# Optimization experiments

Hardware: AMD Instinct MI355X
Metric: run time of the kernel (lower is better)

The kernel has to match this reference:

```python
import jax, jax.numpy as jnp
import numpy as np

NEG = jnp.float32(-1e30)  # log-semiring 'zero' (avoid -inf for safe grads)


def _ctc_total_scores(log_probs, targets, input_lengths, target_lengths):
    """Log-semiring forward over the composed CTC topology.

    log_probs: (T, N, C) log-softmax outputs, blank id = 0
    targets:   (N*L,) flat labels in [1, C)
    Returns tot_scores (N,): log p(targets | log_probs) per utterance,
    identical to k2.intersect_dense + get_tot_scores(log_semiring=True).
    """
    T, N, C = log_probs.shape
    L = targets.shape[0] // N
    tgt = targets.reshape(N, L).astype(jnp.int32)
    S = 2 * L + 1  # extended sequence: blank y1 blank y2 ... yL blank

    ext = jnp.zeros((N, S), jnp.int32).at[:, 1::2].set(tgt)
    s_idx = jnp.arange(S)
    # skip transition s-2 -> s allowed only for label states with ext[s] != ext[s-2]
    diff = jnp.concatenate([jnp.zeros((N, 2), bool), ext[:, 2:] != ext[:, :-2]], axis=1)
    skip_ok = (s_idx[None, :] % 2 == 1) & (s_idx[None, :] >= 2) & diff
    # states beyond this utterance's extended length are invalid
    valid = s_idx[None, :] <= 2 * target_lengths.astype(jnp.int32)[:, None]
    s_end = 2 * target_lengths.astype(jnp.int32)  # index of final blank state

    def emit(lp):  # (N, C) -> (N, S): gather log-probs of extended labels
        return jnp.take_along_axis(lp, ext, axis=1)

    e0 = emit(log_probs[0])
    a0 = jnp.full((N, S), NEG).at[:, 0].set(e0[:, 0]).at[:, 1].set(e0[:, 1])
    a0 = jnp.where(valid, a0, NEG)

    def final_score(a):  # logsumexp over the two accepting states
        last = jnp.take_along_axis(a, s_end[:, None], axis=1)[:, 0]
        prev = jnp.take_along_axis(a, (s_end - 1)[:, None], axis=1)[:, 0]
        return jnp.logaddexp(last, prev)

    def step(a, lp):
        sh1 = jnp.concatenate([jnp.full((N, 1), NEG), a[:, :-1]], axis=1)
        sh2 = jnp.concatenate([jnp.full((N, 2), NEG), a[:, :-2]], axis=1)
        sh2 = jnp.where(skip_ok, sh2, NEG)
        a_new = jnp.logaddexp(jnp.logaddexp(a, sh1), sh2) + emit(lp)
        a_new = jnp.where(valid, a_new, NEG)
        return a_new, final_score(a_new)

    _, finals = jax.lax.scan(step, a0, log_probs[1:])  # finals: (T-1, N)
    finals = jnp.concatenate([final_score(a0)[None], finals], axis=0)  # (T, N)
    tot = jnp.take_along_axis(finals, (input_lengths.astype(jnp.int32) - 1)[None, :], axis=0)[0]
    return tot


def setup_inputs() -> dict:
    key = jax.random.key(0)
    k1, k2_ = jax.random.split(key)
    T, N, C, L = 1500, 32, 1024, 100
    log_probs = jax.nn.log_softmax(
        jax.random.normal(k1, (T, N, C), dtype=jnp.float32), axis=-1)
    targets = jax.random.randint(k2_, (N * L,), 1, C, dtype=jnp.int32)  # no blanks
    input_lengths = jnp.full((N,), T, dtype=jnp.int32)
    target_lengths = jnp.full((N,), L, dtype=jnp.int32)
    return {"log_probs": log_probs, "targets": targets,
            "input_lengths": input_lengths, "target_lengths": target_lengths}


def reference(log_probs, targets, input_lengths, target_lengths):
    tot = _ctc_total_scores(log_probs, targets, input_lengths, target_lengths)
    # drop -inf (failed) segments like get_tot_objf_and_num_frames, then negate sum
    finite = tot > jnp.float32(-1e29)
    return -jnp.sum(jnp.where(finite, tot, 0.0))
```

## Files before the change

kernel.cpp:

```cpp
#include <hip/hip_runtime.h>
#include <stdint.h>

#define NEGF  (-1e30f)
#define LOG2E 1.4426950408889634f
#define LN2F  0.6931471805599453f

__device__ __forceinline__ float fexp2(float x) {
#if __has_builtin(__builtin_amdgcn_exp2f)
    return __builtin_amdgcn_exp2f(x);
#else
    return exp2f(x);
#endif
}
__device__ __forceinline__ float flog2(float x) {
#if __has_builtin(__builtin_amdgcn_logf)
    return __builtin_amdgcn_logf(x);
#else
    return log2f(x);
#endif
}
__device__ __forceinline__ float lse2(float a, float b) {
    float m  = fmaxf(a, b);
    float mn = fminf(a, b);
    return m + flog2(1.0f + fexp2(mn - m));
}
__device__ __forceinline__ float lse3(float a, float b, float c) {
    float m = fmaxf(fmaxf(a, b), c);
    float s = fexp2(a - m) + fexp2(b - m) + fexp2(c - m);
    return m + flog2(s);
}

__device__ __forceinline__ float dpp_shr1(float x, float fill) {
    int r = __builtin_amdgcn_update_dpp(__float_as_int(fill), __float_as_int(x),
                                        0x138, 0xf, 0xf, false);
    return __int_as_float(r);
}
__device__ __forceinline__ float dpp_shl1(float x, float fill) {
    int r = __builtin_amdgcn_update_dpp(__float_as_int(fill), __float_as_int(x),
                                        0x130, 0xf, 0xf, false);
    return __int_as_float(r);
}

#define RB  16
#define VMW "s_waitcnt vmcnt(52)"

__device__ __forceinline__ void stage_row(const float* __restrict__ src, float* dst)
{
    const int lane = threadIdx.x;
    const float* g = src + (lane << 2);
    __builtin_amdgcn_global_load_lds((const __attribute__((address_space(1))) void*)(g),
        (__attribute__((address_space(3))) void*)(dst), 16, 0, 0);
    __builtin_amdgcn_global_load_lds((const __attribute__((address_space(1))) void*)(g + 256),
        (__attribute__((address_space(3))) void*)(dst + 256), 16, 0, 0);
    __builtin_amdgcn_global_load_lds((const __attribute__((address_space(1))) void*)(g + 512),
        (__attribute__((address_space(3))) void*)(dst + 512), 16, 0, 0);
    __builtin_amdgcn_global_load_lds((const __attribute__((address_space(1))) void*)(g + 768),
        (__attribute__((address_space(3))) void*)(dst + 768), 16, 0, 0);
}

__device__ __forceinline__ void lds_read3(uint32_t sb, uint32_t o1, uint32_t o3,
                                          float& eb, float& e1, float& e3)
{
    asm volatile("s_mov_b32 m0, -1\n\t"
                 "ds_read_b32 %0, %3\n\t"
                 "ds_read_b32 %1, %4\n\t"
                 "ds_read_b32 %2, %5"
                 : "=&v"(eb), "=&v"(e1), "=&v"(e3)
                 : "v"(sb), "v"(sb + o1), "v"(sb + o3)
                 : "memory");
}
__device__ __forceinline__ void lds_read4(uint32_t sb, uint32_t o1, uint32_t o3, uint32_t o5,
                                          float& eb, float& e1, float& e3, float& e5)
{
    asm volatile("s_mov_b32 m0, -1\n\t"
                 "ds_read_b32 %0, %4\n\t"
                 "ds_read_b32 %1, %5\n\t"
                 "ds_read_b32 %2, %6\n\t"
                 "ds_read_b32 %3, %7"
                 : "=&v"(eb), "=&v"(e1), "=&v"(e3), "=&v"(e5)
                 : "v"(sb), "v"(sb + o1), "v"(sb + o3), "v"(sb + o5)
                 : "memory");
}

#define LGKM_WAIT3(c, x0, x1, x2) \
    asm volatile("s_waitcnt lgkmcnt(" #c ")" : "+v"(x0), "+v"(x1), "+v"(x2) :: "memory")
#define LGKM_WAIT4(c, x0, x1, x2, x3) \
    asm volatile("s_waitcnt lgkmcnt(" #c ")" : "+v"(x0), "+v"(x1), "+v"(x2), "+v"(x3) :: "memory")

__global__ __launch_bounds__(64, 1)
void ctc_scan(const float* __restrict__ lp, const int* __restrict__ tgt,
              const int* __restrict__ ilen, const int* __restrict__ tlen,
              float* __restrict__ wsA, float* __restrict__ wsB,
              int T, int N, int C, int L)
{
    __shared__ float ring[RB * 1024];

    const int  b      = blockIdx.x;
    const bool is_fwd = (b < N);
    const int  n      = is_fwd ? b : (b - N);
    const int  lane   = threadIdx.x;
    const int  len_t  = tlen[n];
    const int  len_in = ilen[n];
    const int  tm     = (len_in - 1) >> 1;
    const int  send   = 2 * len_t;

    const long tb = (long)n * L;
    auto getT = [&](int k) -> int {
        return (k >= 0 && k < len_t) ? tgt[tb + k] : 0;
    };
    const int lm1 = getT(2 * lane - 1);
    const int l1  = getT(2 * lane);
    const int l2  = getT(2 * lane + 1);
    const int l3  = getT(2 * lane + 2);
    const uint32_t o1 = (uint32_t)l1 << 2;
    const uint32_t o3 = (uint32_t)l2 << 2;
    const uint32_t o5 = (uint32_t)l3 << 2;
    const bool skip1 = (lane > 0) && (l1 != lm1);
    const bool skip3 = (l2 != l1);
    const bool skip5 = (l3 != l2);
    const int  s0 = 4 * lane;

    const long   rstride = (long)N * C;
    const float* row0    = lp + (long)n * C;
    const uint32_t ringb =
        (uint32_t)(uintptr_t)(const __attribute__((address_space(3))) void*)ring;


    if (is_fwd) {
        float eb0 = row0[0];
        float e10 = row0[l1];
        asm volatile("s_waitcnt vmcnt(0)" : "+v"(eb0), "+v"(e10) :: "memory");
        float a0 = (lane == 0) ? eb0 * LOG2E : NEGF;
        float a1 = (lane == 0 && 1 <= send) ? e10 * LOG2E : NEGF;
        float a2 = NEGF, a3 = NEGF;
        float p3 = NEGF;

        auto fstep = [&](float ebr, float e1r, float e3r) {
            float eb = ebr * LOG2E, e1 = e1r * LOG2E, e3 = e3r * LOG2E;
            float n0 = lse2(a0, p3) + eb;
            float n1 = lse3(a1, a0, skip1 ? p3 : NEGF) + e1;
            float n2 = lse2(a2, a1) + eb;
            float n3 = lse3(a3, a2, skip3 ? a1 : NEGF) + e3;
            a0 = n0; a1 = n1; a2 = n2; a3 = n3;
            p3 = dpp_shr1(a3, NEGF);
        };

        const int nsteps = tm;
        const int lim    = len_in - 1;
        for (int j = 0; j < RB - 1; ++j) {
            int r = 1 + j; if (r > lim) r = lim;
            stage_row(row0 + (long)r * rstride, ring + (j << 10));
        }
        asm volatile(VMW ::: "memory");
        float ebA, e1A, e3A, ebB, e1B, e3B;
        lds_read3(ringb,        o1, o3, ebA, e1A, e3A);
        lds_read3(ringb + 4096, o1, o3, ebB, e1B, e3B);

        int i = 0;
        for (; i + 1 < nsteps; i += 2) {
            {   int s = i + RB - 1; int r = s + 1; if (r > lim) r = lim;
                stage_row(row0 + (long)r * rstride, ring + ((s & (RB - 1)) << 10)); }
            LGKM_WAIT3(3, ebA, e1A, e3A);
            fstep(ebA, e1A, e3A);
            asm volatile(VMW ::: "memory");
            lds_read3(ringb + (uint32_t)(((i + 2) & (RB - 1)) << 12), o1, o3,
                      ebA, e1A, e3A);

            {   int s = i + RB; int r = s + 1; if (r > lim) r = lim;
                stage_row(row0 + (long)r * rstride, ring + ((s & (RB - 1)) << 10)); }
            LGKM_WAIT3(3, ebB, e1B, e3B);
            fstep(ebB, e1B, e3B);
            asm volatile(VMW ::: "memory");
            lds_read3(ringb + (uint32_t)(((i + 3) & (RB - 1)) << 12), o1, o3,
                      ebB, e1B, e3B);
        }
        if (i < nsteps) {
            LGKM_WAIT3(0, ebA, e1A, e3A);
            fstep(ebA, e1A, e3A);
        }
        asm volatile("s_waitcnt vmcnt(0) lgkmcnt(0)" ::: "memory");
        *((float4*)(wsA + (long)n * 256) + lane) = make_float4(a0, a1, a2, a3);
    } else {
        float b0 = (s0     == send || s0     == send - 1) ? 0.0f : NEGF;
        float b1 = (s0 + 1 == send || s0 + 1 == send - 1) ? 0.0f : NEGF;
        float b2 = (s0 + 2 == send || s0 + 2 == send - 1) ? 0.0f : NEGF;
        float b3 = (s0 + 3 == send || s0 + 3 == send - 1) ? 0.0f : NEGF;
        float q0 = dpp_shl1(b0, NEGF);
        float q1 = dpp_shl1(b1, NEGF);

        auto bstep = [&](float ebr, float e1r, float e3r, float e5r) {
            float ebl = ebr * LOG2E, e1l = e1r * LOG2E;
            float e3l = e3r * LOG2E, e5l = e5r * LOG2E;
            float f0 = b0 + ebl;
            float f1 = b1 + e1l;
            float f2 = b2 + ebl;
            float f3 = b3 + e3l;
            float f0p = q0 + ebl;
            float f1p = q1 + e5l;
            b0 = lse2(f0, f1);
            b1 = lse3(f1, f2, skip3 ? f3 : NEGF);
            b2 = lse2(f2, f3);
            b3 = lse3(f3, f0p, skip5 ? f1p : NEGF);
            q0 = dpp_shl1(b0, NEGF);
            q1 = dpp_shl1(b1, NEGF);
        };

        const int nsteps = len_in - 1 - tm;
        asm volatile("s_waitcnt vmcnt(0)" ::: "memory");
        for (int j = 0; j < RB - 1; ++j) {
            int r = len_in - 1 - j; if (r < 0) r = 0;
            stage_row(row0 + (long)r * rstride, ring + (j << 10));
        }
        asm volatile(VMW ::: "memory");
        float ebA, e1A, e3A, e5A, ebB, e1B, e3B, e5B;
        lds_read4(ringb,        o1, o3, o5, ebA, e1A, e3A, e5A);
        lds_read4(ringb + 4096, o1, o3, o5, ebB, e1B, e3B, e5B);

        int i = 0;
        for (; i + 1 < nsteps; i += 2) {
            {   int s = i + RB - 1; int r = len_in - 1 - s; if (r < 0) r = 0;
                stage_row(row0 + (long)r * rstride, ring + ((s & (RB - 1)) << 10)); }
            LGKM_WAIT4(4, ebA, e1A, e3A, e5A);
            bstep(ebA, e1A, e3A, e5A);
            asm volatile(VMW ::: "memory");
            lds_read4(ringb + (uint32_t)(((i + 2) & (RB - 1)) << 12), o1, o3, o5,
                      ebA, e1A, e3A, e5A);

            {   int s = i + RB; int r = len_in - 1 - s; if (r < 0) r = 0;
                stage_row(row0 + (long)r * rstride, ring + ((s & (RB - 1)) << 10)); }
            LGKM_WAIT4(4, ebB, e1B, e3B, e5B);
            bstep(ebB, e1B, e3B, e5B);
            asm volatile(VMW ::: "memory");
            lds_read4(ringb + (uint32_t)(((i + 3) & (RB - 1)) << 12), o1, o3, o5,
                      ebB, e1B, e3B, e5B);
        }
        if (i < nsteps) {
            LGKM_WAIT4(0, ebA, e1A, e3A, e5A);
            bstep(ebA, e1A, e3A, e5A);
        }
        asm volatile("s_waitcnt vmcnt(0) lgkmcnt(0)" ::: "memory");
        *((float4*)(wsB + (long)n * 256) + lane) = make_float4(b0, b1, b2, b3);
    }
}

__global__ __launch_bounds__(64, 1)
void ctc_combine(const float* __restrict__ wsA, const float* __restrict__ wsB,
                 float* __restrict__ out)
{
    const int n = blockIdx.x;
    const int lane = threadIdx.x;
    const float4 A = *((const float4*)(wsA + (long)n * 256) + lane);
    const float4 B = *((const float4*)(wsB + (long)n * 256) + lane);
    float v = lse2(lse2(A.x + B.x, A.y + B.y), lse2(A.z + B.z, A.w + B.w));
    #pragma unroll
    for (int off = 1; off < 64; off <<= 1) {
        float o = __shfl_xor(v, off, 64);
        v = lse2(v, o);
    }
    if (lane == 0) {
        float tot = v * LN2F;
        if (tot > -1e29f) atomicAdd(out, -tot);
    }
}

extern "C" void kernel_launch(void* const* d_in, const int* in_sizes, int n_in,
                              void* d_out, int out_size, void* d_ws, size_t ws_size,
                              hipStream_t stream) {
    const float* lp      = (const float*)d_in[0];
    const int*   targets = (const int*)d_in[1];
    const int*   in_len  = (const int*)d_in[2];
    const int*   tgt_len = (const int*)d_in[3];
    const int N = in_sizes[2];
    const int L = in_sizes[1] / N;
    const int C = 1024;
    const int T = (int)((long)in_sizes[0] / ((long)N * C));

    float* out = (float*)d_out;
    float* wsA = (float*)d_ws;
    float* wsB = wsA + (long)N * 256;

    hipMemsetAsync(out, 0, sizeof(float), stream);
    ctc_scan<<<2 * N, 64, 0, stream>>>(lp, targets, in_len, tgt_len,
                                       wsA, wsB, T, N, C, L);
    ctc_combine<<<N, 64, 0, stream>>>(wsA, wsB, out);
}
```

Measured before the change: 336.6 us.

## Switch CTC scan from log-domain to scaled linear-domain recurrence with periodic renorm

Replaces the per-step log-sum-exp recurrences with linear-probability arithmetic. Emissions are normalised by the blank emission, the blank log-probs are accumulated in double, and the state is rescaled every 8 steps with per-lane power-of-two exponent tracking passed across lanes via DPP. This removes most exp/log transcendentals from the serial critical path. The ring pipeline is also deepened to four LDS reads in flight, with a 16-step unroll and an adjusted vmcnt threshold. The trade-off is more complex exponent bookkeeping and a risk of underflow or precision loss between renormalisations.

```diff
diff --git a/kernel.cpp b/kernel.cpp
--- a/kernel.cpp
+++ b/kernel.cpp
@@ -24,11 +24,6 @@
     float mn = fminf(a, b);
     return m + flog2(1.0f + fexp2(mn - m));
 }
-__device__ __forceinline__ float lse3(float a, float b, float c) {
-    float m = fmaxf(fmaxf(a, b), c);
-    float s = fexp2(a - m) + fexp2(b - m) + fexp2(c - m);
-    return m + flog2(s);
-}
 
 __device__ __forceinline__ float dpp_shr1(float x, float fill) {
     int r = __builtin_amdgcn_update_dpp(__float_as_int(fill), __float_as_int(x),
@@ -42,9 +37,9 @@
 }
 
 #define RB  16
-#define VMW "s_waitcnt vmcnt(52)"
-
-__device__ __forceinline__ void stage_row(const float* __restrict__ src, float* dst)
+#define VMW "s_waitcnt vmcnt(44)"
+
+__device__ __forceinline__ void stage_row_c(const float* src, float* dst)
 {
     const int lane = threadIdx.x;
     const float* g = src + (lane << 2);
@@ -86,6 +81,24 @@
     asm volatile("s_waitcnt lgkmcnt(" #c ")" : "+v"(x0), "+v"(x1), "+v"(x2) :: "memory")
 #define LGKM_WAIT4(c, x0, x1, x2, x3) \
     asm volatile("s_waitcnt lgkmcnt(" #c ")" : "+v"(x0), "+v"(x1), "+v"(x2), "+v"(x3) :: "memory")
+
+#define RENORM_LANE(x0, x1, x2, x3, DPPC)                                     \
+  do {                                                                        \
+    float m_ = fmaxf(fmaxf(x0, x1), fmaxf(x2, x3));                           \
+    int   ei_ = (__float_as_int(m_) >> 23) & 0xff;                            \
+    bool  z_  = (m_ == 0.0f);                                                 \
+    float sc_ = z_ ? 1.0f : ((ei_ != 0) ? __int_as_float((254 - ei_) << 23)   \
+                                        : __int_as_float(253 << 23));         \
+    int   d_  = z_ ? 0 : ((ei_ != 0) ? (ei_ - 127) : -126);                   \
+    int   eu_ = esum + d_;                                                    \
+    int   en_ = __builtin_amdgcn_update_dpp(eu_, eu_, (DPPC), 0xf, 0xf, false);\
+    esum = z_ ? en_ : eu_;                          \
+    x0 *= sc_; x1 *= sc_; x2 *= sc_; x3 *= sc_;                               \
+    int   ep_ = __builtin_amdgcn_update_dpp(esum, esum, (DPPC), 0xf, 0xf, false);\
+    int   ce_ = ep_ - esum;                                                   \
+    ce_ = ce_ < -126 ? -126 : (ce_ > 126 ? 126 : ce_);                        \
+    cross = __int_as_float((ce_ + 127) << 23);                                \
+  } while (0)
 
 __global__ __launch_bounds__(64, 1)
 void ctc_scan(const float* __restrict__ lp, const int* __restrict__ tgt,
@@ -125,121 +138,192 @@
     const uint32_t ringb =
         (uint32_t)(uintptr_t)(const __attribute__((address_space(3))) void*)ring;
 
+    int    esum  = 0;
+    float  cross = 1.0f;
+    double dsum  = 0.0;
 
     if (is_fwd) {
         float eb0 = row0[0];
         float e10 = row0[l1];
         asm volatile("s_waitcnt vmcnt(0)" : "+v"(eb0), "+v"(e10) :: "memory");
-        float a0 = (lane == 0) ? eb0 * LOG2E : NEGF;
-        float a1 = (lane == 0 && 1 <= send) ? e10 * LOG2E : NEGF;
-        float a2 = NEGF, a3 = NEGF;
-        float p3 = NEGF;
-
-        auto fstep = [&](float ebr, float e1r, float e3r) {
-            float eb = ebr * LOG2E, e1 = e1r * LOG2E, e3 = e3r * LOG2E;
-            float n0 = lse2(a0, p3) + eb;
-            float n1 = lse3(a1, a0, skip1 ? p3 : NEGF) + e1;
-            float n2 = lse2(a2, a1) + eb;
-            float n3 = lse3(a3, a2, skip3 ? a1 : NEGF) + e3;
-            a0 = n0; a1 = n1; a2 = n2; a3 = n3;
-            p3 = dpp_shr1(a3, NEGF);
-        };
+        dsum = (double)eb0;
+        float a0 = (lane == 0) ? 1.0f : 0.0f;
+        float a1 = (lane == 0 && 1 <= send) ? fexp2((e10 - eb0) * LOG2E) : 0.0f;
+        float a2 = 0.0f, a3 = 0.0f;
+        float p3 = 0.0f;
 
         const int nsteps = tm;
         const int lim    = len_in - 1;
         for (int j = 0; j < RB - 1; ++j) {
             int r = 1 + j; if (r > lim) r = lim;
-            stage_row(row0 + (long)r * rstride, ring + (j << 10));
-        }
+            stage_row_c(row0 + (long)r * rstride, ring + (j << 10));
+        }
+        int rr = (16 > lim) ? lim : 16;
+        const float* pstage = row0 + (long)rr * rstride;
+
         asm volatile(VMW ::: "memory");
-        float ebA, e1A, e3A, ebB, e1B, e3B;
-        lds_read3(ringb,        o1, o3, ebA, e1A, e3A);
-        lds_read3(ringb + 4096, o1, o3, ebB, e1B, e3B);
+        float rb0, r1_0, r3_0, rb1, r1_1, r3_1;
+        float rb2, r1_2, r3_2, rb3, r1_3, r3_3;
+        lds_read3(ringb,         o1, o3, rb0, r1_0, r3_0);
+        lds_read3(ringb + 4096,  o1, o3, rb1, r1_1, r3_1);
+        lds_read3(ringb + 8192,  o1, o3, rb2, r1_2, r3_2);
+        lds_read3(ringb + 12288, o1, o3, rb3, r1_3, r3_3);
+
+#define FSLOT(u, s)                                                            \
+  do {                                                                         \
+    stage_row_c(pstage, ring + ((((u) + 15) & 15) << 10));                     \
+    { int adv = (rr < lim); rr += adv; pstage += adv ? rstride : 0; }          \
+    asm volatile(VMW ::: "memory");                                            \
+    LGKM_WAIT3(9, rb##s, r1_##s, r3_##s);                                      \
+    float cb = rb##s, c1v = r1_##s, c3v = r3_##s;                              \
+    lds_read3(ringb + ((((u) + 4) & 15) << 12), o1, o3, rb##s, r1_##s, r3_##s);\
+    float rv1 = fexp2((c1v - cb) * LOG2E);                                     \
+    float rv3 = fexp2((c3v - cb) * LOG2E);                                     \
+    dsum += (double)cb;                                                        \
+    float n0 = a0 + p3;                                                        \
+    float n1 = (a1 + a0 + (skip1 ? p3 : 0.0f)) * rv1;                          \
+    float n2 = a2 + a1;                                                        \
+    float n3 = (a3 + a2 + (skip3 ? a1 : 0.0f)) * rv3;                          \
+    a0 = n0; a1 = n1; a2 = n2; a3 = n3;                                        \
+    p3 = dpp_shr1(a3, 0.0f) * cross;                                           \
+  } while (0)
+
+#define RENORM_F() do { RENORM_LANE(a0, a1, a2, a3, 0x138);                    \
+                        p3 = dpp_shr1(a3, 0.0f) * cross; } while (0)
 
         int i = 0;
-        for (; i + 1 < nsteps; i += 2) {
-            {   int s = i + RB - 1; int r = s + 1; if (r > lim) r = lim;
-                stage_row(row0 + (long)r * rstride, ring + ((s & (RB - 1)) << 10)); }
-            LGKM_WAIT3(3, ebA, e1A, e3A);
-            fstep(ebA, e1A, e3A);
-            asm volatile(VMW ::: "memory");
-            lds_read3(ringb + (uint32_t)(((i + 2) & (RB - 1)) << 12), o1, o3,
-                      ebA, e1A, e3A);
-
-            {   int s = i + RB; int r = s + 1; if (r > lim) r = lim;
-                stage_row(row0 + (long)r * rstride, ring + ((s & (RB - 1)) << 10)); }
-            LGKM_WAIT3(3, ebB, e1B, e3B);
-            fstep(ebB, e1B, e3B);
-            asm volatile(VMW ::: "memory");
-            lds_read3(ringb + (uint32_t)(((i + 3) & (RB - 1)) << 12), o1, o3,
-                      ebB, e1B, e3B);
-        }
-        if (i < nsteps) {
-            LGKM_WAIT3(0, ebA, e1A, e3A);
-            fstep(ebA, e1A, e3A);
-        }
-        asm volatile("s_waitcnt vmcnt(0) lgkmcnt(0)" ::: "memory");
-        *((float4*)(wsA + (long)n * 256) + lane) = make_float4(a0, a1, a2, a3);
+        while (i + 16 <= nsteps) {
+            FSLOT(0,0);  FSLOT(1,1);  FSLOT(2,2);  FSLOT(3,3);
+            FSLOT(4,0);  FSLOT(5,1);  FSLOT(6,2);  FSLOT(7,3);
+            RENORM_F();
+            FSLOT(8,0);  FSLOT(9,1);  FSLOT(10,2); FSLOT(11,3);
+            FSLOT(12,0); FSLOT(13,1); FSLOT(14,2); FSLOT(15,3);
+            RENORM_F();
+            i += 16;
+        }
+        asm volatile("s_waitcnt vmcnt(0) lgkmcnt(0)"
+                     :: "v"(rb0), "v"(r1_0), "v"(r3_0), "v"(rb1), "v"(r1_1), "v"(r3_1),
+                        "v"(rb2), "v"(r1_2), "v"(r3_2), "v"(rb3), "v"(r1_3), "v"(r3_3)
+                     : "memory");
+        for (; i < nsteps; ++i) {
+            float cb, c1v, c3v;
+            lds_read3(ringb + (uint32_t)((i & 15) << 12), o1, o3, cb, c1v, c3v);
+            LGKM_WAIT3(0, cb, c1v, c3v);
+            float rv1 = fexp2((c1v - cb) * LOG2E);
+            float rv3 = fexp2((c3v - cb) * LOG2E);
+            dsum += (double)cb;
+            float n0 = a0 + p3;
+            float n1 = (a1 + a0 + (skip1 ? p3 : 0.0f)) * rv1;
+            float n2 = a2 + a1;
+            float n3 = (a3 + a2 + (skip3 ? a1 : 0.0f)) * rv3;
+            a0 = n0; a1 = n1; a2 = n2; a3 = n3;
+            p3 = dpp_shr1(a3, 0.0f) * cross;
+            if ((i & 7) == 7) RENORM_F();
+        }
+        float S  = (float)(dsum * 1.4426950408889634);
+        float fe = (float)esum;
+        float w0 = fmaxf(flog2(a0) + fe + S, NEGF);
+        float w1 = fmaxf(flog2(a1) + fe + S, NEGF);
+        float w2 = fmaxf(flog2(a2) + fe + S, NEGF);
+        float w3 = fmaxf(flog2(a3) + fe + S, NEGF);
+        *((float4*)(wsA + (long)n * 256) + lane) = make_float4(w0, w1, w2, w3);
+#undef FSLOT
+#undef RENORM_F
     } else {
-        float b0 = (s0     == send || s0     == send - 1) ? 0.0f : NEGF;
-        float b1 = (s0 + 1 == send || s0 + 1 == send - 1) ? 0.0f : NEGF;
-        float b2 = (s0 + 2 == send || s0 + 2 == send - 1) ? 0.0f : NEGF;
-        float b3 = (s0 + 3 == send || s0 + 3 == send - 1) ? 0.0f : NEGF;
-        float q0 = dpp_shl1(b0, NEGF);
-        float q1 = dpp_shl1(b1, NEGF);
-
-        auto bstep = [&](float ebr, float e1r, float e3r, float e5r) {
-            float ebl = ebr * LOG2E, e1l = e1r * LOG2E;
-            float e3l = e3r * LOG2E, e5l = e5r * LOG2E;
-            float f0 = b0 + ebl;
-            float f1 = b1 + e1l;
-            float f2 = b2 + ebl;
-            float f3 = b3 + e3l;
-            float f0p = q0 + ebl;
-            float f1p = q1 + e5l;
-            b0 = lse2(f0, f1);
-            b1 = lse3(f1, f2, skip3 ? f3 : NEGF);
-            b2 = lse2(f2, f3);
-            b3 = lse3(f3, f0p, skip5 ? f1p : NEGF);
-            q0 = dpp_shl1(b0, NEGF);
-            q1 = dpp_shl1(b1, NEGF);
-        };
+        float b0 = (s0     == send || s0     == send - 1) ? 1.0f : 0.0f;
+        float b1 = (s0 + 1 == send || s0 + 1 == send - 1) ? 1.0f : 0.0f;
+        float b2 = (s0 + 2 == send || s0 + 2 == send - 1) ? 1.0f : 0.0f;
+        float b3 = (s0 + 3 == send || s0 + 3 == send - 1) ? 1.0f : 0.0f;
+        float q0 = dpp_shl1(b0, 0.0f);
+        float q1 = dpp_shl1(b1, 0.0f);
 
         const int nsteps = len_in - 1 - tm;
-        asm volatile("s_waitcnt vmcnt(0)" ::: "memory");
         for (int j = 0; j < RB - 1; ++j) {
             int r = len_in - 1 - j; if (r < 0) r = 0;
-            stage_row(row0 + (long)r * rstride, ring + (j << 10));
-        }
+            stage_row_c(row0 + (long)r * rstride, ring + (j << 10));
+        }
+        int rr = len_in - 16; if (rr < 0) rr = 0;
+        const float* pstage = row0 + (long)rr * rstride;
+
         asm volatile(VMW ::: "memory");
-        float ebA, e1A, e3A, e5A, ebB, e1B, e3B, e5B;
-        lds_read4(ringb,        o1, o3, o5, ebA, e1A, e3A, e5A);
-        lds_read4(ringb + 4096, o1, o3, o5, ebB, e1B, e3B, e5B);
+        float rb0, r1_0, r3_0, r5_0, rb1, r1_1, r3_1, r5_1;
+        float rb2, r1_2, r3_2, r5_2, rb3, r1_3, r3_3, r5_3;
+        lds_read4(ringb,         o1, o3, o5, rb0, r1_0, r3_0, r5_0);
+        lds_read4(ringb + 4096,  o1, o3, o5, rb1, r1_1, r3_1, r5_1);
+        lds_read4(ringb + 8192,  o1, o3, o5, rb2, r1_2, r3_2, r5_2);
+        lds_read4(ringb + 12288, o1, o3, o5, rb3, r1_3, r3_3, r5_3);
+
+#define BSLOT(u, s)                                                            \
+  do {                                                                         \
+    stage_row_c(pstage, ring + ((((u) + 15) & 15) << 10));                     \
+    { int adv = (rr > 0); rr -= adv; pstage -= adv ? rstride : 0; }            \
+    asm volatile(VMW ::: "memory");                                            \
+    LGKM_WAIT4(12, rb##s, r1_##s, r3_##s, r5_##s);                             \
+    float cb = rb##s, c1v = r1_##s, c3v = r3_##s, c5v = r5_##s;                \
+    lds_read4(ringb + ((((u) + 4) & 15) << 12), o1, o3, o5,                    \
+              rb##s, r1_##s, r3_##s, r5_##s);                                  \
+    float rv1 = fexp2((c1v - cb) * LOG2E);                                     \
+    float rv3 = fexp2((c3v - cb) * LOG2E);                                     \
+    float rv5 = fexp2((c5v - cb) * LOG2E);                                     \
+    dsum += (double)cb;                                                        \
+    float g1 = b1 * rv1, g3 = b3 * rv3;                                        \
+    float n0 = b0 + g1;                                                        \
+    float n1 = g1 + b2 + (skip3 ? g3 : 0.0f);                                  \
+    float n2 = b2 + g3;                                                        \
+    float n3 = g3 + q0 + (skip5 ? q1 * rv5 : 0.0f);                            \
+    b0 = n0; b1 = n1; b2 = n2; b3 = n3;                                        \
+    q0 = dpp_shl1(b0, 0.0f) * cross;                                           \
+    q1 = dpp_shl1(b1, 0.0f) * cross;                                           \
+  } while (0)
+
+#define RENORM_B() do { RENORM_LANE(b0, b1, b2, b3, 0x130);                    \
+                        q0 = dpp_shl1(b0, 0.0f) * cross;                       \
+                        q1 = dpp_shl1(b1, 0.0f) * cross; } while (0)
 
         int i = 0;
-        for (; i + 1 < nsteps; i += 2) {
-            {   int s = i + RB - 1; int r = len_in - 1 - s; if (r < 0) r = 0;
-                stage_row(row0 + (long)r * rstride, ring + ((s & (RB - 1)) << 10)); }
-            LGKM_WAIT4(4, ebA, e1A, e3A, e5A);
-            bstep(ebA, e1A, e3A, e5A);
-            asm volatile(VMW ::: "memory");
-            lds_read4(ringb + (uint32_t)(((i + 2) & (RB - 1)) << 12), o1, o3, o5,
-                      ebA, e1A, e3A, e5A);
-
-            {   int s = i + RB; int r = len_in - 1 - s; if (r < 0) r = 0;
-                stage_row(row0 + (long)r * rstride, ring + ((s & (RB - 1)) << 10)); }
-            LGKM_WAIT4(4, ebB, e1B, e3B, e5B);
-            bstep(ebB, e1B, e3B, e5B);
-            asm volatile(VMW ::: "memory");
-            lds_read4(ringb + (uint32_t)(((i + 3) & (RB - 1)) << 12), o1, o3, o5,
-                      ebB, e1B, e3B, e5B);
-        }
-        if (i < nsteps) {
-            LGKM_WAIT4(0, ebA, e1A, e3A, e5A);
-            bstep(ebA, e1A, e3A, e5A);
-        }
-        asm volatile("s_waitcnt vmcnt(0) lgkmcnt(0)" ::: "memory");
-        *((float4*)(wsB + (long)n * 256) + lane) = make_float4(b0, b1, b2, b3);
+        while (i + 16 <= nsteps) {
+            BSLOT(0,0);  BSLOT(1,1);  BSLOT(2,2);  BSLOT(3,3);
+            BSLOT(4,0);  BSLOT(5,1);  BSLOT(6,2);  BSLOT(7,3);
+            RENORM_B();
+            BSLOT(8,0);  BSLOT(9,1);  BSLOT(10,2); BSLOT(11,3);
+            BSLOT(12,0); BSLOT(13,1); BSLOT(14,2); BSLOT(15,3);
+            RENORM_B();
+            i += 16;
+        }
+        asm volatile("s_waitcnt vmcnt(0) lgkmcnt(0)"
+                     :: "v"(rb0), "v"(r1_0), "v"(r3_0), "v"(r5_0),
+                        "v"(rb1), "v"(r1_1), "v"(r3_1), "v"(r5_1),
+                        "v"(rb2), "v"(r1_2), "v"(r3_2), "v"(r5_2),
+                        "v"(rb3), "v"(r1_3), "v"(r3_3), "v"(r5_3)
+                     : "memory");
+        for (; i < nsteps; ++i) {
+            float cb, c1v, c3v, c5v;
+            lds_read4(ringb + (uint32_t)((i & 15) << 12), o1, o3, o5,
+                      cb, c1v, c3v, c5v);
+            LGKM_WAIT4(0, cb, c1v, c3v, c5v);
+            float rv1 = fexp2((c1v - cb) * LOG2E);
+            float rv3 = fexp2((c3v - cb) * LOG2E);
+            float rv5 = fexp2((c5v - cb) * LOG2E);
+            dsum += (double)cb;
+            float g1 = b1 * rv1, g3 = b3 * rv3;
+            float n0 = b0 + g1;
+            float n1 = g1 + b2 + (skip3 ? g3 : 0.0f);
+            float n2 = b2 + g3;
+            float n3 = g3 + q0 + (skip5 ? q1 * rv5 : 0.0f);
+            b0 = n0; b1 = n1; b2 = n2; b3 = n3;
+            q0 = dpp_shl1(b0, 0.0f) * cross;
+            q1 = dpp_shl1(b1, 0.0f) * cross;
+            if ((i & 7) == 7) RENORM_B();
+        }
+        float S  = (float)(dsum * 1.4426950408889634);
+        float fe = (float)esum;
+        float w0 = fmaxf(flog2(b0) + fe + S, NEGF);
+        float w1 = fmaxf(flog2(b1) + fe + S, NEGF);
+        float w2 = fmaxf(flog2(b2) + fe + S, NEGF);
+        float w3 = fmaxf(flog2(b3) + fe + S, NEGF);
+        *((float4*)(wsB + (long)n * 256) + lane) = make_float4(w0, w1, w2, w3);
+#undef BSLOT
+#undef RENORM_B
     }
 }
 
```

Measured after the change: 319.9 us. 5.0% less time.
